# Performance work log

Measured on AMD Instinct MI355X. Metric: run time of the kernel, lower is better.

Reference implementation:

```python
import jax, jax.numpy as jnp
import numpy as np
from jax import lax

WIN = 11
NUM_CLASSES = 2
WEIGHTS = (1.0, 0.5)
PAD = (WIN - 1) // 2


def _edge_kernel():
    w = -jnp.ones((1, 1, WIN, WIN), jnp.float32)
    return w.at[0, 0, WIN // 2, WIN // 2].set(WIN * WIN - 1.0)


def setup_inputs() -> dict:
    key = jax.random.key(0)
    k0, k1, k2 = jax.random.split(key, 3)
    B, H, W = 16, 1024, 1024
    score0 = jax.random.normal(k0, (B, NUM_CLASSES, H, W), jnp.float32)
    score1 = jax.random.normal(k1, (B, NUM_CLASSES, H, W), jnp.float32)
    target = jax.random.randint(k2, (B, 1, H, W), 0, NUM_CLASSES, jnp.int32)
    return {"score0": score0, "score1": score1, "target": target}


def _loss_one(x, onehot, edge_mask, smoothing):
    # x: [B,C,H,W] logits; onehot: [B,C,H,W]; edge_mask: [B,1,H,W]
    log_p = jax.nn.log_softmax(x, axis=1)
    alpha = smoothing
    # softlabel: filled with alpha, target class gets 1 - alpha + alpha/C
    soft = alpha + onehot * (1.0 - 2.0 * alpha + alpha / NUM_CLASSES)
    mask = onehot * (1.0 - edge_mask) + soft * edge_mask
    # sum over class dim, mean over (B,H,W), negated
    return -jnp.mean(jnp.sum(mask * log_p, axis=1))


def reference(score0, score1, target):
    tgt_f = target.astype(jnp.float32)  # [B,1,H,W]
    edge = lax.conv_general_dilated(
        tgt_f, _edge_kernel(), window_strides=(1, 1),
        padding=((PAD, PAD), (PAD, PAD)),
        dimension_numbers=("NCHW", "OIHW", "NCHW"))
    edge_mask = (edge != 0).astype(jnp.float32)          # [B,1,H,W]
    smoothing = jnp.minimum(jnp.mean(edge_mask), 0.2)
    cls = jnp.arange(NUM_CLASSES, dtype=jnp.int32).reshape(1, NUM_CLASSES, 1, 1)
    onehot = (target == cls).astype(jnp.float32)         # [B,C,H,W]
    loss = (WEIGHTS[0] * _loss_one(score0, onehot, edge_mask, smoothing)
            + WEIGHTS[1] * _loss_one(score1, onehot, edge_mask, smoothing))
    return loss
```

## Files before the change

kernel.cpp:

```cpp
#include <hip/hip_runtime.h>

#define HW_SZ   (1024*1024)
#define NPIX    16777216.0
#define GROUPS  (16*1024*1024/4)
#define PAIRS   (GROUPS/2)

#define TW   128
#define TH   32
#define HALO 5
#define TIW  (TW + 2*HALO)
#define TIH  (TH + 2*HALO)
#define TB_P 144
#define VS_P 142
#define NBX  8
#define NBY  32
#define NBZ  16
#define NB1  (NBX*NBY*NBZ)

#define NB2  2048

#define PACKED_BYTES (GROUPS)
#define WS_NEEDED (PACKED_BYTES + NB1*4 + 4*NB2*4)

__global__ __launch_bounds__(256)
void edge_pack(const int* __restrict__ target,
               unsigned char* __restrict__ packed,
               float* __restrict__ cntpart) {
    __shared__ unsigned char  tb[TIH][TB_P];
    __shared__ unsigned short vs[TH][VS_P];
    __shared__ float          red[4];

    const int tid   = threadIdx.x;
    const int tileX = blockIdx.x * TW;
    const int tileY = blockIdx.y * TH;
    const int b     = blockIdx.z;
    const int bid   = (blockIdx.z * NBY + blockIdx.y) * NBX + blockIdx.x;

    const int* tgt = target + (size_t)b * HW_SZ;

    for (int idx = tid; idx < TIH * TIW; idx += 256) {
        int rr = idx / TIW;
        int cc = idx - rr * TIW;
        int gr = tileY + rr - HALO;
        int gc = tileX + cc - HALO;
        unsigned char v = 0;
        if ((unsigned)gr < 1024u && (unsigned)gc < 1024u)
            v = (unsigned char)tgt[gr * 1024 + gc];
        tb[rr][cc] = v;
    }
    __syncthreads();

    if (tid < TIW) {
        int acc = 0;
        #pragma unroll
        for (int rr = 0; rr < 11; ++rr) acc += tb[rr][tid];
        vs[0][tid] = (unsigned short)acc;
        for (int r = 1; r < TH; ++r) {
            acc += (int)tb[r + 10][tid] - (int)tb[r - 1][tid];
            vs[r][tid] = (unsigned short)acc;
        }
    }
    __syncthreads();

    const int tx = tid & 31;
    const int ty = tid >> 5;

    int cnt = 0;
    #pragma unroll
    for (int p = 0; p < 4; ++p) {
        const int r  = ty + p * 8;
        const int gr = tileY + r;
        const int c0 = tx * 4;

        int S[4];
        int s = 0;
        #pragma unroll
        for (int k = 0; k < 11; ++k) s += vs[r][c0 + k];
        S[0] = s;
        #pragma unroll
        for (int j = 1; j < 4; ++j) {
            s += (int)vs[r][c0 + 10 + j] - (int)vs[r][c0 + j - 1];
            S[j] = s;
        }

        unsigned int pk = 0;
        #pragma unroll
        for (int j = 0; j < 4; ++j) {
            const int t = tb[r + 5][c0 + 5 + j];
            const int e = (S[j] != 121 * t) ? 1 : 0;
            cnt += e;
            pk |= (unsigned)(t << (2 * j)) | (unsigned)(e << (2 * j + 1));
        }
        packed[((size_t)b << 18) + (gr << 8) + (tileX >> 2) + tx] = (unsigned char)pk;
    }

    float v = (float)cnt;
    #pragma unroll
    for (int off = 32; off > 0; off >>= 1) v += __shfl_down(v, off);
    const int lane = tid & 63, wv = tid >> 6;
    if (lane == 0) red[wv] = v;
    __syncthreads();
    if (tid == 0) cntpart[bid] = red[0] + red[1] + red[2] + red[3];
}

__device__ __forceinline__ void px_term(float p0, float p1, int t, float e,
                                        float& s1, float& s2) {
    float m   = fmaxf(p0, p1);
    float lse = m + __logf(1.0f + __expf(-fabsf(p0 - p1)));
    float lpt = (t ? p1 : p0) - lse;
    float slp = p0 + p1 - 2.0f * lse;
    s1 += lpt;
    s2 += e * (slp - 1.5f * lpt);
}

__global__ __launch_bounds__(256)
void loss_stream(const float* __restrict__ score0,
                 const float* __restrict__ score1,
                 const unsigned char* __restrict__ packed,
                 float* __restrict__ spart) {
    const int tid = threadIdx.x;
    const unsigned short* pk16 = (const unsigned short*)packed;

    float a1 = 0.f, a2 = 0.f, b1 = 0.f, b2 = 0.f;

    for (int pp = blockIdx.x * 256 + tid; pp < PAIRS; pp += NB2 * 256) {
        const int b = pp >> 17;
        const size_t off = ((size_t)pp << 3) + ((size_t)b << 20);

        float4 x0a = *(const float4*)(score0 + off);
        float4 x0b = *(const float4*)(score0 + off + 4);
        float4 x1a = *(const float4*)(score0 + off + HW_SZ);
        float4 x1b = *(const float4*)(score0 + off + HW_SZ + 4);
        float4 y0a = *(const float4*)(score1 + off);
        float4 y0b = *(const float4*)(score1 + off + 4);
        float4 y1a = *(const float4*)(score1 + off + HW_SZ);
        float4 y1b = *(const float4*)(score1 + off + HW_SZ + 4);
        const unsigned int pk = pk16[pp];

        float p0[8] = {x0a.x, x0a.y, x0a.z, x0a.w, x0b.x, x0b.y, x0b.z, x0b.w};
        float p1[8] = {x1a.x, x1a.y, x1a.z, x1a.w, x1b.x, x1b.y, x1b.z, x1b.w};
        float q0[8] = {y0a.x, y0a.y, y0a.z, y0a.w, y0b.x, y0b.y, y0b.z, y0b.w};
        float q1[8] = {y1a.x, y1a.y, y1a.z, y1a.w, y1b.x, y1b.y, y1b.z, y1b.w};

        #pragma unroll
        for (int j = 0; j < 8; ++j) {
            const int   t = (pk >> (2 * j)) & 1;
            const float e = (float)((pk >> (2 * j + 1)) & 1);
            px_term(p0[j], p1[j], t, e, a1, a2);
            px_term(q0[j], q1[j], t, e, b1, b2);
        }
    }

    __shared__ float red[4][4];
    float vals[4] = {a1, a2, b1, b2};
    const int lane = tid & 63, wv = tid >> 6;
    #pragma unroll
    for (int q = 0; q < 4; ++q) {
        float v = vals[q];
        #pragma unroll
        for (int off = 32; off > 0; off >>= 1) v += __shfl_down(v, off);
        if (lane == 0) red[wv][q] = v;
    }
    __syncthreads();
    if (tid == 0) {
        #pragma unroll
        for (int q = 0; q < 4; ++q)
            spart[q * NB2 + blockIdx.x] = red[0][q] + red[1][q] + red[2][q] + red[3][q];
    }
}

__global__ __launch_bounds__(256)
void finalize2(const float* __restrict__ cntpart,
               const float* __restrict__ spart,
               float* __restrict__ out) {
    __shared__ double red[4][5];
    const int tid = threadIdx.x;
    double acc[5] = {0, 0, 0, 0, 0};
    for (int i = tid; i < NB1; i += 256) acc[0] += (double)cntpart[i];
    for (int i = tid; i < NB2; i += 256) {
        #pragma unroll
        for (int q = 0; q < 4; ++q) acc[q + 1] += (double)spart[q * NB2 + i];
    }
    const int lane = tid & 63, wv = tid >> 6;
    #pragma unroll
    for (int q = 0; q < 5; ++q) {
        double v = acc[q];
        #pragma unroll
        for (int off = 32; off > 0; off >>= 1) v += __shfl_down(v, off);
        if (lane == 0) red[wv][q] = v;
    }
    __syncthreads();
    if (tid == 0) {
        double s[5];
        #pragma unroll
        for (int q = 0; q < 5; ++q)
            s[q] = red[0][q] + red[1][q] + red[2][q] + red[3][q];
        double alpha = s[0] / NPIX;
        if (alpha > 0.2) alpha = 0.2;
        double loss = (s[1] + alpha * s[2]) + 0.5 * (s[3] + alpha * s[4]);
        out[0] = (float)(-loss / NPIX);
    }
}

__global__ __launch_bounds__(256)
void fused_edge_loss(const float* __restrict__ score0,
                     const float* __restrict__ score1,
                     const int*   __restrict__ target,
                     float*       __restrict__ ws) {
    __shared__ unsigned char  tb[TIH][TB_P];
    __shared__ unsigned short vs[TH][VS_P];
    __shared__ float          red[4][5];

    const int tid   = threadIdx.x;
    const int tileX = blockIdx.x * TW;
    const int tileY = blockIdx.y * TH;
    const int b     = blockIdx.z;
    const int bid   = (blockIdx.z * NBY + blockIdx.y) * NBX + blockIdx.x;

    const int* tgt = target + (size_t)b * HW_SZ;

    for (int idx = tid; idx < TIH * TIW; idx += 256) {
        int rr = idx / TIW;
        int cc = idx - rr * TIW;
        int gr = tileY + rr - HALO;
        int gc = tileX + cc - HALO;
        unsigned char v = 0;
        if ((unsigned)gr < 1024u && (unsigned)gc < 1024u)
            v = (unsigned char)tgt[gr * 1024 + gc];
        tb[rr][cc] = v;
    }
    __syncthreads();

    if (tid < TIW) {
        int acc = 0;
        #pragma unroll
        for (int rr = 0; rr < 11; ++rr) acc += tb[rr][tid];
        vs[0][tid] = (unsigned short)acc;
        for (int r = 1; r < TH; ++r) {
            acc += (int)tb[r + 10][tid] - (int)tb[r - 1][tid];
            vs[r][tid] = (unsigned short)acc;
        }
    }
    __syncthreads();

    const float* s0b = score0 + (size_t)b * (2 * HW_SZ);
    const float* s1b = score1 + (size_t)b * (2 * HW_SZ);
    const int tx = tid & 31;
    const int ty = tid >> 5;

    float cnt = 0.f, a1 = 0.f, a2 = 0.f, b1 = 0.f, b2 = 0.f;

    #pragma unroll
    for (int p = 0; p < 4; ++p) {
        const int r  = ty + p * 8;
        const int gr = tileY + r;
        const int c0 = tx * 4;
        const int gc = tileX + c0;

        int S[4];
        int s = 0;
        #pragma unroll
        for (int k = 0; k < 11; ++k) s += vs[r][c0 + k];
        S[0] = s;
        #pragma unroll
        for (int j = 1; j < 4; ++j) {
            s += (int)vs[r][c0 + 10 + j] - (int)vs[r][c0 + j - 1];
            S[j] = s;
        }

        const size_t base = (size_t)gr * 1024 + gc;
        float4 x0 = *(const float4*)(s0b + base);
        float4 x1 = *(const float4*)(s0b + HW_SZ + base);
        float4 y0 = *(const float4*)(s1b + base);
        float4 y1 = *(const float4*)(s1b + HW_SZ + base);
        float p0a[4] = {x0.x, x0.y, x0.z, x0.w};
        float p1a[4] = {x1.x, x1.y, x1.z, x1.w};
        float q0a[4] = {y0.x, y0.y, y0.z, y0.w};
        float q1a[4] = {y1.x, y1.y, y1.z, y1.w};

        #pragma unroll
        for (int j = 0; j < 4; ++j) {
            const int t = tb[r + 5][c0 + 5 + j];
            const float e = (S[j] != 121 * t) ? 1.0f : 0.0f;
            cnt += e;
            px_term(p0a[j], p1a[j], t, e, a1, a2);
            px_term(q0a[j], q1a[j], t, e, b1, b2);
        }
    }

    float vals[5] = {cnt, a1, a2, b1, b2};
    const int lane = tid & 63, wv = tid >> 6;
    #pragma unroll
    for (int q = 0; q < 5; ++q) {
        float v = vals[q];
        #pragma unroll
        for (int off = 32; off > 0; off >>= 1) v += __shfl_down(v, off);
        if (lane == 0) red[wv][q] = v;
    }
    __syncthreads();
    if (tid == 0) {
        #pragma unroll
        for (int q = 0; q < 5; ++q)
            ws[q * NB1 + bid] = red[0][q] + red[1][q] + red[2][q] + red[3][q];
    }
}

__global__ __launch_bounds__(256)
void finalize_loss(const float* __restrict__ ws, float* __restrict__ out) {
    __shared__ double red[4][5];
    const int tid = threadIdx.x;
    double acc[5] = {0, 0, 0, 0, 0};
    for (int i = tid; i < NB1; i += 256) {
        #pragma unroll
        for (int q = 0; q < 5; ++q) acc[q] += (double)ws[q * NB1 + i];
    }
    const int lane = tid & 63, wv = tid >> 6;
    #pragma unroll
    for (int q = 0; q < 5; ++q) {
        double v = acc[q];
        #pragma unroll
        for (int off = 32; off > 0; off >>= 1) v += __shfl_down(v, off);
        if (lane == 0) red[wv][q] = v;
    }
    __syncthreads();
    if (tid == 0) {
        double s[5];
        #pragma unroll
        for (int q = 0; q < 5; ++q)
            s[q] = red[0][q] + red[1][q] + red[2][q] + red[3][q];
        double alpha = s[0] / NPIX;
        if (alpha > 0.2) alpha = 0.2;
        double loss = (s[1] + alpha * s[2]) + 0.5 * (s[3] + alpha * s[4]);
        out[0] = (float)(-loss / NPIX);
    }
}

extern "C" void kernel_launch(void* const* d_in, const int* in_sizes, int n_in,
                              void* d_out, int out_size, void* d_ws, size_t ws_size,
                              hipStream_t stream) {
    const float* score0 = (const float*)d_in[0];
    const float* score1 = (const float*)d_in[1];
    const int*   target = (const int*)d_in[2];
    float* out = (float*)d_out;

    if (ws_size >= (size_t)WS_NEEDED) {
        unsigned char* packed  = (unsigned char*)d_ws;
        float*         cntpart = (float*)((char*)d_ws + PACKED_BYTES);
        float*         spart   = cntpart + NB1;

        dim3 grid1(NBX, NBY, NBZ);
        edge_pack<<<grid1, 256, 0, stream>>>(target, packed, cntpart);
        loss_stream<<<NB2, 256, 0, stream>>>(score0, score1, packed, spart);
        finalize2<<<1, 256, 0, stream>>>(cntpart, spart, out);
    } else {
        float* ws = (float*)d_ws;
        dim3 grid(NBX, NBY, NBZ);
        fused_edge_loss<<<grid, 256, 0, stream>>>(score0, score1, target, ws);
        finalize_loss<<<1, 256, 0, stream>>>(ws, out);
    }
}
```

Before: 348.2 us.

## Replace box-sum edge detection with bit-plane OR/AND dilation and erosion

Target labels are first packed into one bit per pixel. The edge mask is then computed with 64-bit shift/OR/AND window operations: a pixel is an edge iff its 11x11 window is not uniform, which is OR-dilation and not AND-erosion. The loss stream reads separate target and edge bit planes and now uses 1024-thread blocks, each handling exactly two 8-pixel groups. This is meant to shrink the edge-stage shared-memory and sum work and the packed intermediate traffic, at the cost of an extra kernel launch and correctness that relies on binary labels (it uses v&1).

Measured after the change: 414.6 us. 19.1% more time.

```diff
diff --git a/kernel.cpp b/kernel.cpp
--- a/kernel.cpp
+++ b/kernel.cpp
@@ -1,15 +1,197 @@
 #include <hip/hip_runtime.h>
 
-#define HW_SZ   (1024*1024)
-#define NPIX    16777216.0
-#define GROUPS  (16*1024*1024/4)
-#define PAIRS   (GROUPS/2)
+typedef unsigned long long u64;
+typedef unsigned int       u32;
+
+#define HW_SZ     (1024*1024)
+#define NPIX      16777216.0
+#define WPI       16384
+#define TOTAL_W   (16*WPI)
+#define GROUPS8   (2*1024*1024)
+#define NB2       1024
+#define NBE       256
+#define ETH       4
+
+#define WS_NEEDED (4*1024*1024 + NBE*4 + 4*NB2*4)
+
+__global__ __launch_bounds__(256, 4)
+void bitpack(const int* __restrict__ target, u64* __restrict__ tplane) {
+    const int w = blockIdx.x * 256 + threadIdx.x;
+    const int4* p = (const int4*)(target + ((size_t)w << 6));
+    u64 m = 0;
+    #pragma unroll
+    for (int k = 0; k < 16; ++k) {
+        int4 v = p[k];
+        u32 nib = (u32)(v.x & 1) | ((u32)(v.y & 1) << 1) |
+                  ((u32)(v.z & 1) << 2) | ((u32)(v.w & 1) << 3);
+        m |= (u64)nib << (4 * k);
+    }
+    tplane[w] = m;
+}
+
+__global__ __launch_bounds__(256)
+void edge_bits(const u64* __restrict__ tplane, u64* __restrict__ eplane,
+               float* __restrict__ cntpart) {
+    const int tid = threadIdx.x;
+    const int img = tid >> 4;
+    const int wc  = tid & 15;
+    const int r0  = blockIdx.x * ETH;
+    const u64* base = tplane + ((size_t)img << 14) + wc;
+
+    u64 hor[ETH + 10], hand[ETH + 10];
+    #pragma unroll
+    for (int i = 0; i < ETH + 10; ++i) {
+        const int r = r0 - 5 + i;
+        if ((unsigned)r < 1024u) {
+            const u64* rp = base + r * 16;
+            u64 mw = rp[0];
+            u64 lw = (wc != 0)  ? rp[-1] : 0ull;
+            u64 rw = (wc != 15) ? rp[ 1] : 0ull;
+            u64 o = mw, a = mw;
+            #pragma unroll
+            for (int k = 1; k <= 5; ++k) {
+                u64 rt = (mw >> k) | (rw << (64 - k));
+                u64 lt = (mw << k) | (lw >> (64 - k));
+                o |= rt | lt;
+                a &= rt & lt;
+            }
+            hor[i] = o; hand[i] = a;
+        } else {
+            hor[i] = 0ull; hand[i] = 0ull;
+        }
+    }
+
+    int cnt = 0;
+    #pragma unroll
+    for (int j = 0; j < ETH; ++j) {
+        u64 o = hor[j], a = hand[j];
+        #pragma unroll
+        for (int i = 1; i < 11; ++i) { o |= hor[j + i]; a &= hand[j + i]; }
+        const u64 e = o & ~a;
+        cnt += __popcll(e);
+        eplane[((size_t)img << 14) + (size_t)(r0 + j) * 16 + wc] = e;
+    }
+
+    __shared__ float red[4];
+    float v = (float)cnt;
+    #pragma unroll
+    for (int off = 32; off > 0; off >>= 1) v += __shfl_down(v, off);
+    const int lane = tid & 63, wv = tid >> 6;
+    if (lane == 0) red[wv] = v;
+    __syncthreads();
+    if (tid == 0) cntpart[blockIdx.x] = red[0] + red[1] + red[2] + red[3];
+}
+
+__device__ __forceinline__ void px_term(float p0, float p1, int t, float e,
+                                        float& s1, float& s2) {
+    float m   = fmaxf(p0, p1);
+    float lse = m + __logf(1.0f + __expf(-fabsf(p0 - p1)));
+    float lpt = (t ? p1 : p0) - lse;
+    float slp = p0 + p1 - 2.0f * lse;
+    s1 += lpt;
+    s2 += e * (slp - 1.5f * lpt);
+}
+
+__global__ __launch_bounds__(1024, 8)
+void loss_stream(const float* __restrict__ score0,
+                 const float* __restrict__ score1,
+                 const unsigned char* __restrict__ tb,
+                 const unsigned char* __restrict__ eb,
+                 float* __restrict__ spart) {
+    const int tid = threadIdx.x;
+    float a1 = 0.f, a2 = 0.f, b1 = 0.f, b2 = 0.f;
+
+    #pragma unroll
+    for (int k = 0; k < 2; ++k) {
+        const int g   = blockIdx.x * 2048 + k * 1024 + tid;
+        const int img = g >> 17;
+        const size_t off = ((size_t)img << 21) + ((size_t)(g & 131071) << 3);
+
+        float4 x0a = *(const float4*)(score0 + off);
+        float4 x0b = *(const float4*)(score0 + off + 4);
+        float4 x1a = *(const float4*)(score0 + off + HW_SZ);
+        float4 x1b = *(const float4*)(score0 + off + HW_SZ + 4);
+        float4 y0a = *(const float4*)(score1 + off);
+        float4 y0b = *(const float4*)(score1 + off + 4);
+        float4 y1a = *(const float4*)(score1 + off + HW_SZ);
+        float4 y1b = *(const float4*)(score1 + off + HW_SZ + 4);
+        const u32 t8 = tb[g];
+        const u32 e8 = eb[g];
+
+        float p0[8] = {x0a.x, x0a.y, x0a.z, x0a.w, x0b.x, x0b.y, x0b.z, x0b.w};
+        float p1[8] = {x1a.x, x1a.y, x1a.z, x1a.w, x1b.x, x1b.y, x1b.z, x1b.w};
+        float q0[8] = {y0a.x, y0a.y, y0a.z, y0a.w, y0b.x, y0b.y, y0b.z, y0b.w};
+        float q1[8] = {y1a.x, y1a.y, y1a.z, y1a.w, y1b.x, y1b.y, y1b.z, y1b.w};
+
+        #pragma unroll
+        for (int j = 0; j < 8; ++j) {
+            const int   t = (t8 >> j) & 1;
+            const float e = (float)((e8 >> j) & 1);
+            px_term(p0[j], p1[j], t, e, a1, a2);
+            px_term(q0[j], q1[j], t, e, b1, b2);
+        }
+    }
+
+    __shared__ float red[16][4];
+    float vals[4] = {a1, a2, b1, b2};
+    const int lane = tid & 63, wv = tid >> 6;
+    #pragma unroll
+    for (int q = 0; q < 4; ++q) {
+        float v = vals[q];
+        #pragma unroll
+        for (int off = 32; off > 0; off >>= 1) v += __shfl_down(v, off);
+        if (lane == 0) red[wv][q] = v;
+    }
+    __syncthreads();
+    if (tid == 0) {
+        #pragma unroll
+        for (int q = 0; q < 4; ++q) {
+            float v = 0.f;
+            #pragma unroll
+            for (int w = 0; w < 16; ++w) v += red[w][q];
+            spart[q * NB2 + blockIdx.x] = v;
+        }
+    }
+}
+
+__global__ __launch_bounds__(256)
+void finalize2(const float* __restrict__ cntpart,
+               const float* __restrict__ spart,
+               float* __restrict__ out) {
+    __shared__ double red[4][5];
+    const int tid = threadIdx.x;
+    double acc[5] = {0, 0, 0, 0, 0};
+    for (int i = tid; i < NBE; i += 256) acc[0] += (double)cntpart[i];
+    for (int i = tid; i < NB2; i += 256) {
+        #pragma unroll
+        for (int q = 0; q < 4; ++q) acc[q + 1] += (double)spart[q * NB2 + i];
+    }
+    const int lane = tid & 63, wv = tid >> 6;
+    #pragma unroll
+    for (int q = 0; q < 5; ++q) {
+        double v = acc[q];
+        #pragma unroll
+        for (int off = 32; off > 0; off >>= 1) v += __shfl_down(v, off);
+        if (lane == 0) red[wv][q] = v;
+    }
+    __syncthreads();
+    if (tid == 0) {
+        double s[5];
+        #pragma unroll
+        for (int q = 0; q < 5; ++q)
+            s[q] = red[0][q] + red[1][q] + red[2][q] + red[3][q];
+        double alpha = s[0] / NPIX;
+        if (alpha > 0.2) alpha = 0.2;
+        double loss = (s[1] + alpha * s[2]) + 0.5 * (s[3] + alpha * s[4]);
+        out[0] = (float)(-loss / NPIX);
+    }
+}
 
 #define TW   128
-#define TH   32
+#define FTH  32
 #define HALO 5
 #define TIW  (TW + 2*HALO)
-#define TIH  (TH + 2*HALO)
+#define TIH  (FTH + 2*HALO)
 #define TB_P 144
 #define VS_P 142
 #define NBX  8
@@ -17,22 +199,18 @@
 #define NBZ  16
 #define NB1  (NBX*NBY*NBZ)
 
-#define NB2  2048
-
-#define PACKED_BYTES (GROUPS)
-#define WS_NEEDED (PACKED_BYTES + NB1*4 + 4*NB2*4)
-
 __global__ __launch_bounds__(256)
-void edge_pack(const int* __restrict__ target,
-               unsigned char* __restrict__ packed,
-               float* __restrict__ cntpart) {
-    __shared__ unsigned char  tb[TIH][TB_P];
-    __shared__ unsigned short vs[TH][VS_P];
-    __shared__ float          red[4];
+void fused_edge_loss(const float* __restrict__ score0,
+                     const float* __restrict__ score1,
+                     const int*   __restrict__ target,
+                     float*       __restrict__ ws) {
+    __shared__ unsigned char  tbuf[TIH][TB_P];
+    __shared__ unsigned short vs[FTH][VS_P];
+    __shared__ float          red[4][5];
 
     const int tid   = threadIdx.x;
     const int tileX = blockIdx.x * TW;
-    const int tileY = blockIdx.y * TH;
+    const int tileY = blockIdx.y * FTH;
     const int b     = blockIdx.z;
     const int bid   = (blockIdx.z * NBY + blockIdx.y) * NBX + blockIdx.x;
 
@@ -46,198 +224,17 @@
         unsigned char v = 0;
         if ((unsigned)gr < 1024u && (unsigned)gc < 1024u)
             v = (unsigned char)tgt[gr * 1024 + gc];
-        tb[rr][cc] = v;
+        tbuf[rr][cc] = v;
     }
     __syncthreads();
 
     if (tid < TIW) {
         int acc = 0;
         #pragma unroll
-        for (int rr = 0; rr < 11; ++rr) acc += tb[rr][tid];
+        for (int rr = 0; rr < 11; ++rr) acc += tbuf[rr][tid];
         vs[0][tid] = (unsigned short)acc;
-        for (int r = 1; r < TH; ++r) {
-            acc += (int)tb[r + 10][tid] - (int)tb[r - 1][tid];
-            vs[r][tid] = (unsigned short)acc;
-        }
-    }
-    __syncthreads();
-
-    const int tx = tid & 31;
-    const int ty = tid >> 5;
-
-    int cnt = 0;
-    #pragma unroll
-    for (int p = 0; p < 4; ++p) {
-        const int r  = ty + p * 8;
-        const int gr = tileY + r;
-        const int c0 = tx * 4;
-
-        int S[4];
-        int s = 0;
-        #pragma unroll
-        for (int k = 0; k < 11; ++k) s += vs[r][c0 + k];
-        S[0] = s;
-        #pragma unroll
-        for (int j = 1; j < 4; ++j) {
-            s += (int)vs[r][c0 + 10 + j] - (int)vs[r][c0 + j - 1];
-            S[j] = s;
-        }
-
-        unsigned int pk = 0;
-        #pragma unroll
-        for (int j = 0; j < 4; ++j) {
-            const int t = tb[r + 5][c0 + 5 + j];
-            const int e = (S[j] != 121 * t) ? 1 : 0;
-            cnt += e;
-            pk |= (unsigned)(t << (2 * j)) | (unsigned)(e << (2 * j + 1));
-        }
-        packed[((size_t)b << 18) + (gr << 8) + (tileX >> 2) + tx] = (unsigned char)pk;
-    }
-
-    float v = (float)cnt;
-    #pragma unroll
-    for (int off = 32; off > 0; off >>= 1) v += __shfl_down(v, off);
-    const int lane = tid & 63, wv = tid >> 6;
-    if (lane == 0) red[wv] = v;
-    __syncthreads();
-    if (tid == 0) cntpart[bid] = red[0] + red[1] + red[2] + red[3];
-}
-
-__device__ __forceinline__ void px_term(float p0, float p1, int t, float e,
-                                        float& s1, float& s2) {
-    float m   = fmaxf(p0, p1);
-    float lse = m + __logf(1.0f + __expf(-fabsf(p0 - p1)));
-    float lpt = (t ? p1 : p0) - lse;
-    float slp = p0 + p1 - 2.0f * lse;
-    s1 += lpt;
-    s2 += e * (slp - 1.5f * lpt);
-}
-
-__global__ __launch_bounds__(256)
-void loss_stream(const float* __restrict__ score0,
-                 const float* __restrict__ score1,
-                 const unsigned char* __restrict__ packed,
-                 float* __restrict__ spart) {
-    const int tid = threadIdx.x;
-    const unsigned short* pk16 = (const unsigned short*)packed;
-
-    float a1 = 0.f, a2 = 0.f, b1 = 0.f, b2 = 0.f;
-
-    for (int pp = blockIdx.x * 256 + tid; pp < PAIRS; pp += NB2 * 256) {
-        const int b = pp >> 17;
-        const size_t off = ((size_t)pp << 3) + ((size_t)b << 20);
-
-        float4 x0a = *(const float4*)(score0 + off);
-        float4 x0b = *(const float4*)(score0 + off + 4);
-        float4 x1a = *(const float4*)(score0 + off + HW_SZ);
-        float4 x1b = *(const float4*)(score0 + off + HW_SZ + 4);
-        float4 y0a = *(const float4*)(score1 + off);
-        float4 y0b = *(const float4*)(score1 + off + 4);
-        float4 y1a = *(const float4*)(score1 + off + HW_SZ);
-        float4 y1b = *(const float4*)(score1 + off + HW_SZ + 4);
-        const unsigned int pk = pk16[pp];
-
-        float p0[8] = {x0a.x, x0a.y, x0a.z, x0a.w, x0b.x, x0b.y, x0b.z, x0b.w};
-        float p1[8] = {x1a.x, x1a.y, x1a.z, x1a.w, x1b.x, x1b.y, x1b.z, x1b.w};
-        float q0[8] = {y0a.x, y0a.y, y0a.z, y0a.w, y0b.x, y0b.y, y0b.z, y0b.w};
-        float q1[8] = {y1a.x, y1a.y, y1a.z, y1a.w, y1b.x, y1b.y, y1b.z, y1b.w};
-
-        #pragma unroll
-        for (int j = 0; j < 8; ++j) {
-            const int   t = (pk >> (2 * j)) & 1;
-            const float e = (float)((pk >> (2 * j + 1)) & 1);
-            px_term(p0[j], p1[j], t, e, a1, a2);
-            px_term(q0[j], q1[j], t, e, b1, b2);
-        }
-    }
-
-    __shared__ float red[4][4];
-    float vals[4] = {a1, a2, b1, b2};
-    const int lane = tid & 63, wv = tid >> 6;
-    #pragma unroll
-    for (int q = 0; q < 4; ++q) {
-        float v = vals[q];
-        #pragma unroll
-        for (int off = 32; off > 0; off >>= 1) v += __shfl_down(v, off);
-        if (lane == 0) red[wv][q] = v;
-    }
-    __syncthreads();
-    if (tid == 0) {
-        #pragma unroll
-        for (int q = 0; q < 4; ++q)
-            spart[q * NB2 + blockIdx.x] = red[0][q] + red[1][q] + red[2][q] + red[3][q];
-    }
-}
-
-__global__ __launch_bounds__(256)
-void finalize2(const float* __restrict__ cntpart,
-               const float* __restrict__ spart,
-               float* __restrict__ out) {
-    __shared__ double red[4][5];
-    const int tid = threadIdx.x;
-    double acc[5] = {0, 0, 0, 0, 0};
-    for (int i = tid; i < NB1; i += 256) acc[0] += (double)cntpart[i];
-    for (int i = tid; i < NB2; i += 256) {
-        #pragma unroll
-        for (int q = 0; q < 4; ++q) acc[q + 1] += (double)spart[q * NB2 + i];
-    }
-    const int lane = tid & 63, wv = tid >> 6;
-    #pragma unroll
-    for (int q = 0; q < 5; ++q) {
-        double v = acc[q];
-        #pragma unroll
-        for (int off = 32; off > 0; off >>= 1) v += __shfl_down(v, off);
-        if (lane == 0) red[wv][q] = v;
-    }
-    __syncthreads();
-    if (tid == 0) {
-        double s[5];
-        #pragma unroll
-        for (int q = 0; q < 5; ++q)
-            s[q] = red[0][q] + red[1][q] + red[2][q] + red[3][q];
-        double alpha = s[0] / NPIX;
-        if (alpha > 0.2) alpha = 0.2;
-        double loss = (s[1] + alpha * s[2]) + 0.5 * (s[3] + alpha * s[4]);
-        out[0] = (float)(-loss / NPIX);
-    }
-}
-
-__global__ __launch_bounds__(256)
-void fused_edge_loss(const float* __restrict__ score0,
-                     const float* __restrict__ score1,
-                     const int*   __restrict__ target,
-                     float*       __restrict__ ws) {
-    __shared__ unsigned char  tb[TIH][TB_P];
-    __shared__ unsigned short vs[TH][VS_P];
-    __shared__ float          red[4][5];
-
-    const int tid   = threadIdx.x;
-    const int tileX = blockIdx.x * TW;
-    const int tileY = blockIdx.y * TH;
-    const int b     = blockIdx.z;
-    const int bid   = (blockIdx.z * NBY + blockIdx.y) * NBX + blockIdx.x;
-
-    const int* tgt = target + (size_t)b * HW_SZ;
-
-    for (int idx = tid; idx < TIH * TIW; idx += 256) {
-        int rr = idx / TIW;
-        int cc = idx - rr * TIW;
-        int gr = tileY + rr - HALO;
-        int gc = tileX + cc - HALO;
-        unsigned char v = 0;
-        if ((unsigned)gr < 1024u && (unsigned)gc < 1024u)
-            v = (unsigned char)tgt[gr * 1024 + gc];
-        tb[rr][cc] = v;
-    }
-    __syncthreads();
-
-    if (tid < TIW) {
-        int acc = 0;
-        #pragma unroll
-        for (int rr = 0; rr < 11; ++rr) acc += tb[rr][tid];
-        vs[0][tid] = (unsigned short)acc;
-        for (int r = 1; r < TH; ++r) {
-            acc += (int)tb[r + 10][tid] - (int)tb[r - 1][tid];
+        for (int r = 1; r < FTH; ++r) {
+            acc += (int)tbuf[r + 10][tid] - (int)tbuf[r - 1][tid];
             vs[r][tid] = (unsigned short)acc;
         }
     }
@@ -280,7 +277,7 @@
 
         #pragma unroll
         for (int j = 0; j < 4; ++j) {
-            const int t = tb[r + 5][c0 + 5 + j];
+            const int t = tbuf[r + 5][c0 + 5 + j];
             const float e = (S[j] != 121 * t) ? 1.0f : 0.0f;
             cnt += e;
             px_term(p0a[j], p1a[j], t, e, a1, a2);
@@ -344,14 +341,18 @@
     float* out = (float*)d_out;
 
     if (ws_size >= (size_t)WS_NEEDED) {
-        unsigned char* packed  = (unsigned char*)d_ws;
-        float*         cntpart = (float*)((char*)d_ws + PACKED_BYTES);
-        float*         spart   = cntpart + NB1;
-
-        dim3 grid1(NBX, NBY, NBZ);
-        edge_pack<<<grid1, 256, 0, stream>>>(target, packed, cntpart);
-        loss_stream<<<NB2, 256, 0, stream>>>(score0, score1, packed, spart);
-        finalize2<<<1, 256, 0, stream>>>(cntpart, spart, out);
+        u64*   tplane  = (u64*)d_ws;
+        u64*   eplane  = (u64*)((char*)d_ws + 2*1024*1024);
+        float* cntpart = (float*)((char*)d_ws + 4*1024*1024);
+        float* spart   = cntpart + NBE;
+
+        bitpack   <<<TOTAL_W/256, 256, 0, stream>>>(target, tplane);
+        edge_bits <<<1024/ETH,    256, 0, stream>>>(tplane, eplane, cntpart);
+        loss_stream<<<NB2,       1024, 0, stream>>>(score0, score1,
+                                                    (const unsigned char*)tplane,
+                                                    (const unsigned char*)eplane,
+                                                    spart);
+        finalize2 <<<1, 256, 0, stream>>>(cntpart, spart, out);
     } else {
         float* ws = (float*)d_ws;
         dim3 grid(NBX, NBY, NBZ);
```
